# Kernel tuning notes

Measured on AMD Instinct MI355X. Metric: run time of the kernel, lower is better.

## Reference

```python
import jax, jax.numpy as jnp
import numpy as np

N_NODES = 50000
N_EDGES = 800000
IN_CH = 128
HID_CH = 256
N_GRAPHS = 500


def setup_inputs() -> dict:
    key = jax.random.key(0)
    k = jax.random.split(key, 8)
    x = jax.random.normal(k[0], (N_NODES, IN_CH), dtype=jnp.float32)
    edge_index = jax.random.randint(k[1], (2, N_EDGES), 0, N_NODES, dtype=jnp.int32)
    batch = jnp.sort(jax.random.randint(k[2], (N_NODES,), 0, N_GRAPHS, dtype=jnp.int32))
    # GCNConv weights (glorot-ish scaling) and zero biases, Linear fc is unused in forward
    W1 = jax.random.normal(k[3], (IN_CH, HID_CH), dtype=jnp.float32) / np.sqrt(IN_CH)
    b1 = jnp.zeros((HID_CH,), dtype=jnp.float32)
    W2 = jax.random.normal(k[4], (HID_CH, HID_CH), dtype=jnp.float32) / np.sqrt(HID_CH)
    b2 = jnp.zeros((HID_CH,), dtype=jnp.float32)
    return {"x": x, "W1": W1, "b1": b1, "W2": W2, "b2": b2,
            "edge_index": edge_index, "batch": batch}


def _gcn_conv(x, W, b, src, dst, norm, n_nodes):
    # x' = scatter_add_dst( norm_e * (x @ W)[src] ) + b   (self-loops already in src/dst)
    xw = x @ W                              # [N, H]
    msg = xw[src] * norm[:, None]           # [E+N, H]
    out = jax.ops.segment_sum(msg, dst, num_segments=n_nodes)
    return out + b


def reference(x, W1, b1, W2, b2, edge_index, batch):
    n = x.shape[0]
    # add self-loops (PyG GCNConv default)
    loop = jnp.arange(n, dtype=edge_index.dtype)
    src = jnp.concatenate([edge_index[0], loop])
    dst = jnp.concatenate([edge_index[1], loop])
    # symmetric normalization D^{-1/2} (A+I) D^{-1/2}; deg from dst counts
    deg = jax.ops.segment_sum(jnp.ones_like(dst, dtype=x.dtype), dst, num_segments=n)
    dis = jnp.where(deg > 0, jax.lax.rsqrt(deg), 0.0)
    norm = dis[src] * dis[dst]              # [E+N]

    h = jax.nn.relu(_gcn_conv(x, W1, b1, src, dst, norm, n))
    h = jax.nn.relu(_gcn_conv(h, W2, b2, src, dst, norm, n))

    # global_mean_pool over batch ids
    sums = jax.ops.segment_sum(h, batch, num_segments=N_GRAPHS)
    cnts = jax.ops.segment_sum(jnp.ones((n,), dtype=h.dtype), batch, num_segments=N_GRAPHS)
    return sums / jnp.maximum(cnts, 1.0)[:, None]
```

## Files before the change

### kernel.cpp

```cpp
#include <hip/hip_runtime.h>

#define HID 256
#define SLOTS 30
#define OVCAP 16384
#define NB 256
typedef unsigned short ushort_t;
typedef unsigned int uint_t;
typedef __attribute__((ext_vector_type(8))) short short8;
typedef __attribute__((ext_vector_type(4))) float f32x4;
typedef __attribute__((ext_vector_type(4))) unsigned short us4;
typedef __attribute__((ext_vector_type(8))) unsigned short us8;

__device__ __forceinline__ ushort_t f2b(float f) {
    uint_t u = __float_as_uint(f);
    u = u + 0x7fffu + ((u >> 16) & 1u);
    return (ushort_t)(u >> 16);
}

__global__ __launch_bounds__(256) void k_histprep(const int* __restrict__ dst,
                                                  int* __restrict__ hist,
                                                  int E, int CH, int NBKT,
                                                  const float* __restrict__ W1,
                                                  ushort_t* __restrict__ Wt1,
                                                  const float* __restrict__ W2,
                                                  ushort_t* __restrict__ Wt2, int p1b) {
    int bid = blockIdx.x;
    int tid = threadIdx.x;
    if (bid < NB) {
        __shared__ int h[256];
        h[tid] = 0;
        __syncthreads();
        int e0 = bid * CH;
        for (int it = tid; it < CH; it += 256) {
            int e = e0 + it;
            if (e < E) atomicAdd(&h[dst[e] >> 8], 1);
        }
        __syncthreads();
        if (tid < NBKT) hist[tid * NB + bid] = h[tid];
        return;
    }
    const float* W = (bid < NB + p1b) ? W1 : W2;
    ushort_t* Wt = (bid < NB + p1b) ? Wt1 : Wt2;
    int kg = (bid < NB + p1b) ? (bid - NB) : (bid - NB - p1b);
    int c = tid;
    float v = W[(size_t)kg * HID + c];
    int p = kg >> 6;
    int k = kg & 63;
    int byte_ = c * 128 + k * 2;
    int slot = byte_ >> 4;
    int sw = (slot & ~7) | ((slot ^ c) & 7);
    size_t dst_byte = (size_t)p * 32768 + ((size_t)sw << 4) + (byte_ & 15);
    Wt[dst_byte >> 1] = f2b(v);
}

__global__ __launch_bounds__(256) void k_scanb(const int* __restrict__ hist,
                                               int* __restrict__ offb,
                                               int* __restrict__ base,
                                               int* __restrict__ ovn, int NBKT) {
    __shared__ int s[256];
    int t = threadIdx.x;
    int sum = 0;
    if (t < NBKT) {
        const int* hp = hist + t * NB;
        for (int blk = 0; blk < NB; ++blk) sum += hp[blk];
    }
    s[t] = sum;
    __syncthreads();
#pragma unroll
    for (int d = 1; d < 256; d <<= 1) {
        int u = (t >= d) ? s[t - d] : 0;
        __syncthreads();
        s[t] += u;
        __syncthreads();
    }
    int myBase = s[t] - sum;
    if (t < NBKT) {
        base[t] = myBase;
        int run = myBase;
        const int* hp = hist + t * NB;
        int* op = offb + t * NB;
        for (int blk = 0; blk < NB; ++blk) { op[blk] = run; run += hp[blk]; }
    }
    if (t == 255) { base[NBKT] = s[255]; *ovn = 0; }
}

__global__ __launch_bounds__(256) void k_scatter(const int* __restrict__ src,
                                                 const int* __restrict__ dst,
                                                 const int* __restrict__ offb,
                                                 uint_t* __restrict__ scat,
                                                 int E, int CH) {
    __shared__ int h[256];
    int tid = threadIdx.x;
    int bid = blockIdx.x;
    h[tid] = 0;
    __syncthreads();
    int e0 = bid * CH;
    for (int it = tid; it < CH; it += 256) {
        int e = e0 + it;
        if (e < E) {
            int d = dst[e], sv = src[e];
            int b = d >> 8;
            int r = atomicAdd(&h[b], 1);
            scat[offb[b * NB + bid] + r] = ((uint_t)sv << 8) | (uint_t)(d & 255);
        }
    }
}

__global__ __launch_bounds__(256) void k_csr(const uint_t* __restrict__ scat,
                                             const int* __restrict__ base,
                                             ushort_t* __restrict__ csr2,
                                             float* __restrict__ dis,
                                             int* __restrict__ ovn,
                                             int2* __restrict__ ov,
                                             const float* __restrict__ x,
                                             ushort_t* __restrict__ xg, int n) {
    __shared__ ushort_t rows[256 * 32];
    __shared__ int rc[256];
    __shared__ float sdis[256];
    int tid = threadIdx.x;
    int b = blockIdx.x;
    rc[tid] = 0;
    uint4* r4 = (uint4*)rows;
#pragma unroll
    for (int k = tid; k < 1024; k += 256) r4[k] = make_uint4(0u, 0u, 0u, 0u);
    __syncthreads();
    int lo = base[b], hi = base[b + 1];
    for (int i = lo + tid; i < hi; i += 256) {
        uint_t p = scat[i];
        int local = (int)(p & 255u);
        int sv = (int)(p >> 8);
        int c = atomicAdd(&rc[local], 1);
        if (c < SLOTS) {
            rows[local * 32 + c] = (ushort_t)sv;
        } else {
            int q = atomicAdd(ovn, 1);
            if (q < OVCAP) ov[q] = make_int2(b * 256 + local, sv);
        }
    }
    __syncthreads();
    ((int*)(rows + tid * 32))[15] = rc[tid];
    float dv = rsqrtf((float)(rc[tid] + 1));
    sdis[tid] = dv;
    int node = b * 256 + tid;
    if (node < n) dis[node] = dv;
    __syncthreads();
    int node0 = b * 256;
    uint4* cg = (uint4*)csr2;
#pragma unroll
    for (int k = tid; k < 1024; k += 256) {
        int row = k >> 2, word = k & 3;
        if (node0 + row < n) cg[(size_t)(node0 + row) * 4 + word] = r4[row * 4 + word];
    }
#pragma unroll
    for (int c = 0; c < 16; ++c) {
        int u = c * 256 + tid;
        int rl = u >> 4;
        int j = u & 15;
        int node2 = node0 + rl;
        if (node2 < n) {
            float dvv = sdis[rl];
            const float4* p = (const float4*)(x + (size_t)node2 * 128 + j * 8);
            float4 v0 = p[0], v1 = p[1];
            us8 o;
            o[0] = f2b(v0.x * dvv); o[1] = f2b(v0.y * dvv);
            o[2] = f2b(v0.z * dvv); o[3] = f2b(v0.w * dvv);
            o[4] = f2b(v1.x * dvv); o[5] = f2b(v1.y * dvv);
            o[6] = f2b(v1.z * dvv); o[7] = f2b(v1.w * dvv);
            size_t dst = (size_t)(j >> 2) * ((size_t)n * 32) + (size_t)node2 * 32
                         + (size_t)(j & 3) * 8;
            *(us8*)(xg + dst) = o;
        }
    }
}

#define ACC8(r)                                                            \
    a0 += __uint_as_float((r).x << 16); a1 += __uint_as_float((r).x & 0xffff0000u); \
    a2 += __uint_as_float((r).y << 16); a3 += __uint_as_float((r).y & 0xffff0000u); \
    a4 += __uint_as_float((r).z << 16); a5 += __uint_as_float((r).z & 0xffff0000u); \
    a6 += __uint_as_float((r).w << 16); a7 += __uint_as_float((r).w & 0xffff0000u);

#define ACC8B(r)                                                           \
    b0 += __uint_as_float((r).x << 16); b1 += __uint_as_float((r).x & 0xffff0000u); \
    b2 += __uint_as_float((r).y << 16); b3 += __uint_as_float((r).y & 0xffff0000u); \
    b4 += __uint_as_float((r).z << 16); b5 += __uint_as_float((r).z & 0xffff0000u); \
    b6 += __uint_as_float((r).w << 16); b7 += __uint_as_float((r).w & 0xffff0000u);

template <int NG>
__global__ __launch_bounds__(256) void k_agg_g(const ushort_t* __restrict__ Yg,
                                               ushort_t* __restrict__ Z,
                                               const ushort_t* __restrict__ csr2,
                                               const int* __restrict__ ovn,
                                               const int2* __restrict__ ov,
                                               const float* __restrict__ dis, int n) {
    const int LOG = (NG == 8) ? 3 : 2;
    const int g = blockIdx.x & (NG - 1);
    const int chunk = blockIdx.x >> LOG;
    const int q = threadIdx.x >> 4;
    const int l16 = threadIdx.x & 15;
    const int par = l16 >> 2;
    const int sub = l16 & 3;
    const int v0 = chunk * 32 + q * 2;
    if (v0 >= n) return;
    const int v1 = v0 + 1;
    const bool has1 = (v1 < n);
    const uint4* Yb = (const uint4*)(Yg + (size_t)g * ((size_t)n * 32));
    const ushort_t* rowb0 = csr2 + (size_t)v0 * 32;
    const ushort_t* rowb1 = csr2 + (size_t)v1 * 32;
    const int deg0 = ((const int*)rowb0)[15];
    const int deg1 = has1 ? ((const int*)rowb1)[15] : 0;
    const int lim0 = min(deg0, SLOTS);
    const int lim1 = min(deg1, SLOTS);
    const int base = par * 8;
    us8 idx0 = *(const us8*)(rowb0 + base);
    us8 idx1 = {};
    if (has1) idx1 = *(const us8*)(rowb1 + base);
    uint4 self0 = make_uint4(0u, 0u, 0u, 0u), self1 = make_uint4(0u, 0u, 0u, 0u);
    if (par == 0) self0 = Yb[(uint_t)v0 * 4u + sub];
    if (has1 && par == 1) self1 = Yb[(uint_t)v1 * 4u + sub];

    const bool g0 = base < lim0;
    const bool g1 = has1 && (base < lim1);
    uint4 r0, r1, r2, r3, r4, r5, r6, r7;
    uint4 s0, s1, s2, s3, s4, s5, s6, s7;
    if (g0) {
        r0 = Yb[(uint_t)idx0[0] * 4u + sub]; r1 = Yb[(uint_t)idx0[1] * 4u + sub];
        r2 = Yb[(uint_t)idx0[2] * 4u + sub]; r3 = Yb[(uint_t)idx0[3] * 4u + sub];
        r4 = Yb[(uint_t)idx0[4] * 4u + sub]; r5 = Yb[(uint_t)idx0[5] * 4u + sub];
        r6 = Yb[(uint_t)idx0[6] * 4u + sub]; r7 = Yb[(uint_t)idx0[7] * 4u + sub];
    }
    if (g1) {
        s0 = Yb[(uint_t)idx1[0] * 4u + sub]; s1 = Yb[(uint_t)idx1[1] * 4u + sub];
        s2 = Yb[(uint_t)idx1[2] * 4u + sub]; s3 = Yb[(uint_t)idx1[3] * 4u + sub];
        s4 = Yb[(uint_t)idx1[4] * 4u + sub]; s5 = Yb[(uint_t)idx1[5] * 4u + sub];
        s6 = Yb[(uint_t)idx1[6] * 4u + sub]; s7 = Yb[(uint_t)idx1[7] * 4u + sub];
    }
    float a0 = 0.f, a1 = 0.f, a2 = 0.f, a3 = 0.f, a4 = 0.f, a5 = 0.f, a6 = 0.f, a7 = 0.f;
    float b0 = 0.f, b1 = 0.f, b2 = 0.f, b3 = 0.f, b4 = 0.f, b5 = 0.f, b6 = 0.f, b7 = 0.f;
    if (g0) {
        if (base + 0 < lim0) { ACC8(r0); }
        if (base + 1 < lim0) { ACC8(r1); }
        if (base + 2 < lim0) { ACC8(r2); }
        if (base + 3 < lim0) { ACC8(r3); }
        if (base + 4 < lim0) { ACC8(r4); }
        if (base + 5 < lim0) { ACC8(r5); }
        if (base + 6 < lim0) { ACC8(r6); }
        if (base + 7 < lim0) { ACC8(r7); }
    }
    if (g1) {
        if (base + 0 < lim1) { ACC8B(s0); }
        if (base + 1 < lim1) { ACC8B(s1); }
        if (base + 2 < lim1) { ACC8B(s2); }
        if (base + 3 < lim1) { ACC8B(s3); }
        if (base + 4 < lim1) { ACC8B(s4); }
        if (base + 5 < lim1) { ACC8B(s5); }
        if (base + 6 < lim1) { ACC8B(s6); }
        if (base + 7 < lim1) { ACC8B(s7); }
    }
    if (deg0 > SLOTS) {
        int m = min(*ovn, OVCAP);
        for (int i2 = par; i2 < m; i2 += 4) {
            int2 p = ov[i2];
            if (p.x == v0) { uint4 r = Yb[(uint_t)p.y * 4u + sub]; ACC8(r); }
        }
    }
    if (deg1 > SLOTS) {
        int m = min(*ovn, OVCAP);
        for (int i2 = par; i2 < m; i2 += 4) {
            int2 p = ov[i2];
            if (p.x == v1) { uint4 r = Yb[(uint_t)p.y * 4u + sub]; ACC8B(r); }
        }
    }
    a0 += __shfl_xor(a0, 4, 64); a1 += __shfl_xor(a1, 4, 64);
    a2 += __shfl_xor(a2, 4, 64); a3 += __shfl_xor(a3, 4, 64);
    a4 += __shfl_xor(a4, 4, 64); a5 += __shfl_xor(a5, 4, 64);
    a6 += __shfl_xor(a6, 4, 64); a7 += __shfl_xor(a7, 4, 64);
    a0 += __shfl_xor(a0, 8, 64); a1 += __shfl_xor(a1, 8, 64);
    a2 += __shfl_xor(a2, 8, 64); a3 += __shfl_xor(a3, 8, 64);
    a4 += __shfl_xor(a4, 8, 64); a5 += __shfl_xor(a5, 8, 64);
    a6 += __shfl_xor(a6, 8, 64); a7 += __shfl_xor(a7, 8, 64);
    b0 += __shfl_xor(b0, 4, 64); b1 += __shfl_xor(b1, 4, 64);
    b2 += __shfl_xor(b2, 4, 64); b3 += __shfl_xor(b3, 4, 64);
    b4 += __shfl_xor(b4, 4, 64); b5 += __shfl_xor(b5, 4, 64);
    b6 += __shfl_xor(b6, 4, 64); b7 += __shfl_xor(b7, 4, 64);
    b0 += __shfl_xor(b0, 8, 64); b1 += __shfl_xor(b1, 8, 64);
    b2 += __shfl_xor(b2, 8, 64); b3 += __shfl_xor(b3, 8, 64);
    b4 += __shfl_xor(b4, 8, 64); b5 += __shfl_xor(b5, 8, 64);
    b6 += __shfl_xor(b6, 8, 64); b7 += __shfl_xor(b7, 8, 64);
    if (par == 0) {
        ACC8(self0);
        float dv = dis[v0];
        us8 o;
        o[0] = f2b(a0 * dv); o[1] = f2b(a1 * dv); o[2] = f2b(a2 * dv); o[3] = f2b(a3 * dv);
        o[4] = f2b(a4 * dv); o[5] = f2b(a5 * dv); o[6] = f2b(a6 * dv); o[7] = f2b(a7 * dv);
        us8* zp = (us8*)(Z + (size_t)v0 * (NG * 32) + g * 32 + sub * 8);
        __builtin_nontemporal_store(o, zp);
    }
    if (has1 && par == 1) {
        ACC8B(self1);
        float dv = dis[v1];
        us8 o;
        o[0] = f2b(b0 * dv); o[1] = f2b(b1 * dv); o[2] = f2b(b2 * dv); o[3] = f2b(b3 * dv);
        o[4] = f2b(b4 * dv); o[5] = f2b(b5 * dv); o[6] = f2b(b6 * dv); o[7] = f2b(b7 * dv);
        us8* zp = (us8*)(Z + (size_t)v1 * (NG * 32) + g * 32 + sub * 8);
        __builtin_nontemporal_store(o, zp);
    }
}

template <int K, bool SCALE, bool OUTG>
__global__ __launch_bounds__(512) void k_gemm_mfma(const ushort_t* __restrict__ A,
                                                   const ushort_t* __restrict__ Wt,
                                                   const float* __restrict__ dis,
                                                   const float* __restrict__ bias,
                                                   ushort_t* __restrict__ Yout, int M) {
    __shared__ char lds[49152];
    char* As = lds;
    char* Bs = lds + 16384;
    const int tid = threadIdx.x;
    const int lane = tid & 63;
    const int w = tid >> 6;
    const int wm = w & 1;
    const int wn = w >> 1;
    const int row0 = blockIdx.x * 128;

    f32x4 acc[4][4];
#pragma unroll
    for (int i = 0; i < 4; ++i)
#pragma unroll
        for (int j = 0; j < 4; ++j) acc[i][j] = (f32x4){0.f, 0.f, 0.f, 0.f};

    for (int k0 = 0; k0 < K; k0 += 64) {
#pragma unroll
        for (int q = 0; q < 2; ++q) {
            int s = q * 512 + tid;
            int r = s >> 3;
            int kseg = (s & 7) ^ (r & 7);
            int row = row0 + r;
            if (row >= M) row = 0;
            const ushort_t* g = A + (size_t)row * K + k0 + kseg * 8;
            __builtin_amdgcn_global_load_lds((const uint_t*)g,
                                             (uint_t*)(As + q * 8192 + w * 1024), 16, 0, 0);
        }
        const ushort_t* gp = Wt + (size_t)(k0 >> 6) * (256 * 64);
#pragma unroll
        for (int q = 0; q < 4; ++q) {
            int s = q * 512 + tid;
            __builtin_amdgcn_global_load_lds((const uint_t*)(gp + (size_t)s * 8),
                                             (uint_t*)(Bs + q * 8192 + w * 1024), 16, 0, 0);
        }
        __syncthreads();
#pragma unroll
        for (int k32 = 0; k32 < 2; ++k32) {
            const int ksl = k32 * 4 + (lane >> 4);
            short8 wf[4], xf[4];
#pragma unroll
            for (int nn = 0; nn < 4; ++nn) {
                int col = wn * 64 + nn * 16 + (lane & 15);
                int slot = col * 8 + (ksl ^ (col & 7));
                wf[nn] = *(const short8*)(Bs + slot * 16);
            }
#pragma unroll
            for (int m = 0; m < 4; ++m) {
                int row = wm * 64 + m * 16 + (lane & 15);
                int slot = row * 8 + (ksl ^ (row & 7));
                xf[m] = *(const short8*)(As + slot * 16);
            }
#pragma unroll
            for (int nn = 0; nn < 4; ++nn)
#pragma unroll
                for (int m = 0; m < 4; ++m)
                    acc[nn][m] = __builtin_amdgcn_mfma_f32_16x16x32_bf16(wf[nn], xf[m],
                                                                         acc[nn][m], 0, 0, 0);
        }
        __syncthreads();
    }
    const int m_lo = lane & 15, c_hi = lane >> 4;
#pragma unroll
    for (int m = 0; m < 4; ++m) {
        int row = row0 + wm * 64 + m * 16 + m_lo;
        if (row < M) {
            float dv = SCALE ? dis[row] : 1.f;
#pragma unroll
            for (int nn = 0; nn < 4; ++nn) {
                int c0 = wn * 64 + nn * 16 + c_hi * 4;
                float4 bb = *(const float4*)(bias + c0);
                us4 o;
                o[0] = f2b(fmaxf(acc[nn][m][0] + bb.x, 0.f) * dv);
                o[1] = f2b(fmaxf(acc[nn][m][1] + bb.y, 0.f) * dv);
                o[2] = f2b(fmaxf(acc[nn][m][2] + bb.z, 0.f) * dv);
                o[3] = f2b(fmaxf(acc[nn][m][3] + bb.w, 0.f) * dv);
                size_t dst = OUTG
                    ? ((size_t)(c0 >> 5) * ((size_t)M * 32) + (size_t)row * 32 + (c0 & 31))
                    : ((size_t)row * HID + c0);
                *(us4*)(Yout + dst) = o;
            }
        }
    }
}

__global__ __launch_bounds__(256) void k_pool2(const ushort_t* __restrict__ H,
                                               const int* __restrict__ batch,
                                               float* __restrict__ out, int n) {
    __shared__ int se[2];
    int g = blockIdx.x;
    if (threadIdx.x < 2) {
        int tgt = g + (int)threadIdx.x;
        int lo = 0, hi = n;
        while (lo < hi) { int mid = (lo + hi) >> 1; if (batch[mid] < tgt) lo = mid + 1; else hi = mid; }
        se[threadIdx.x] = lo;
    }
    __syncthreads();
    int s = se[0], e = se[1];
    int c = threadIdx.x;
    float sum = 0.f;
    for (int i = s; i < e; ++i)
        sum += __uint_as_float(((uint_t)H[(size_t)i * HID + c]) << 16);
    out[(size_t)g * HID + c] = sum / (float)max(e - s, 1);
}

extern "C" void kernel_launch(void* const* d_in, const int* in_sizes, int n_in,
                              void* d_out, int out_size, void* d_ws, size_t ws_size,
                              hipStream_t stream) {
    const float* x = (const float*)d_in[0];
    const float* W1 = (const float*)d_in[1];
    const float* b1 = (const float*)d_in[2];
    const float* W2 = (const float*)d_in[3];
    const float* b2 = (const float*)d_in[4];
    const int* ei = (const int*)d_in[5];
    const int* batch = (const int*)d_in[6];
    float* out = (float*)d_out;

    const int N = in_sizes[6];
    const int E = in_sizes[5] / 2;
    const int K1 = in_sizes[0] / N;
    const int G = out_size / HID;
    (void)n_in; (void)ws_size; (void)K1;

    char* w = (char*)d_ws;
    int* ovn = (int*)(w + 0);
    int2* ov = (int2*)(w + 64);
    ushort_t* csr2 = (ushort_t*)(w + 131136);
    float* dis = (float*)(w + 3331136);
    ushort_t* Wt1 = (ushort_t*)(w + 3531136);
    ushort_t* Wt2 = (ushort_t*)(w + 3596672);
    ushort_t* Xg = (ushort_t*)(w + 3727744);
    ushort_t* Z1 = (ushort_t*)(w + 16527744);
    ushort_t* H1g = (ushort_t*)(w + 29327744);
    ushort_t* Z2 = (ushort_t*)(w + 3727744);
    ushort_t* H2 = (ushort_t*)(w + 29327744);
    int* hist = (int*)(w + 54927744);
    int* offb = (int*)(w + 55128448);
    int* base = (int*)(w + 55329152);
    uint_t* scat = (uint_t*)(w + 55330048);

    const int NBKT = (N + 255) >> 8;
    const int CH = (E + NB - 1) / NB;
    k_histprep<<<NB + K1 + HID, 256, 0, stream>>>(ei + E, hist, E, CH, NBKT,
                                                  W1, Wt1, W2, Wt2, K1);
    k_scanb<<<1, 256, 0, stream>>>(hist, offb, base, ovn, NBKT);
    k_scatter<<<NB, 256, 0, stream>>>(ei, ei + E, offb, scat, E, CH);
    k_csr<<<NBKT, 256, 0, stream>>>(scat, base, csr2, dis, ovn, ov, x, Xg, N);

    int gblk = (N + 127) / 128;
    const int chunks32 = (N + 31) / 32;
    k_agg_g<4><<<4 * chunks32, 256, 0, stream>>>(Xg, Z1, csr2, ovn, ov, dis, N);
    k_gemm_mfma<128, true, true><<<gblk, 512, 0, stream>>>(Z1, Wt1, dis, b1, H1g, N);
    k_agg_g<8><<<8 * chunks32, 256, 0, stream>>>(H1g, Z2, csr2, ovn, ov, dis, N);
    k_gemm_mfma<256, false, false><<<gblk, 512, 0, stream>>>(Z2, Wt2, dis, b2, H2, N);

    k_pool2<<<G, 256, 0, stream>>>(H2, batch, out, N);
}
```

Before: 202.8 us.

## Sort nodes by degree and process one node per 16-lane group in aggregation

Adds a degree histogram in k_csr plus two new kernels (a scan and a scatter) that build a permutation of nodes sorted into degree bins. The aggregation kernels now handle one node per 16-lane group taken from this permutation, instead of two consecutive nodes per group. The aim is to cut warp divergence and load imbalance from varying degrees, so that lanes in a wave finish at similar times. In exchange it adds launches and an extra indirection through perm, halves the per-thread work, and gives up the locality of consecutive node ids for Z writes and self reads.

```diff
diff --git a/kernel.cpp b/kernel.cpp
--- a/kernel.cpp
+++ b/kernel.cpp
@@ -113,13 +113,16 @@
                                              int* __restrict__ ovn,
                                              int2* __restrict__ ov,
                                              const float* __restrict__ x,
-                                             ushort_t* __restrict__ xg, int n) {
+                                             ushort_t* __restrict__ xg,
+                                             int* __restrict__ dhist, int n) {
     __shared__ ushort_t rows[256 * 32];
     __shared__ int rc[256];
     __shared__ float sdis[256];
+    __shared__ int dh[32];
     int tid = threadIdx.x;
     int b = blockIdx.x;
     rc[tid] = 0;
+    if (tid < 32) dh[tid] = 0;
     uint4* r4 = (uint4*)rows;
 #pragma unroll
     for (int k = tid; k < 1024; k += 256) r4[k] = make_uint4(0u, 0u, 0u, 0u);
@@ -142,8 +145,12 @@
     float dv = rsqrtf((float)(rc[tid] + 1));
     sdis[tid] = dv;
     int node = b * 256 + tid;
-    if (node < n) dis[node] = dv;
-    __syncthreads();
+    if (node < n) {
+        dis[node] = dv;
+        atomicAdd(&dh[min(rc[tid], 31)], 1);
+    }
+    __syncthreads();
+    if (tid < 32) dhist[b * 32 + tid] = dh[tid];
     int node0 = b * 256;
     uint4* cg = (uint4*)csr2;
 #pragma unroll
@@ -173,17 +180,49 @@
     }
 }
 
+__global__ __launch_bounds__(256) void k_dscan(const int* __restrict__ dhist,
+                                               int* __restrict__ doffb, int NBKT) {
+    __shared__ int s[32];
+    int t = threadIdx.x;
+    if (t < 32) {
+        int sum = 0;
+        for (int b = 0; b < NBKT; ++b) sum += dhist[b * 32 + t];
+        s[t] = sum;
+    }
+    __syncthreads();
+    if (t == 0) {
+        int run = 0;
+        for (int d = 0; d < 32; ++d) { int c = s[d]; s[d] = run; run += c; }
+    }
+    __syncthreads();
+    if (t < 32) {
+        int run = s[t];
+        for (int b = 0; b < NBKT; ++b) { doffb[t * NBKT + b] = run; run += dhist[b * 32 + t]; }
+    }
+}
+
+__global__ __launch_bounds__(256) void k_dscat(const ushort_t* __restrict__ csr2,
+                                               const int* __restrict__ doffb,
+                                               int* __restrict__ perm, int n, int NBKT) {
+    __shared__ int dh[32];
+    int tid = threadIdx.x;
+    int b = blockIdx.x;
+    if (tid < 32) dh[tid] = 0;
+    __syncthreads();
+    int node = b * 256 + tid;
+    if (node < n) {
+        int deg = ((const int*)csr2)[node * 16 + 15];
+        int bin = min(deg, 31);
+        int r = atomicAdd(&dh[bin], 1);
+        perm[doffb[bin * NBKT + b] + r] = node;
+    }
+}
+
 #define ACC8(r)                                                            \
     a0 += __uint_as_float((r).x << 16); a1 += __uint_as_float((r).x & 0xffff0000u); \
     a2 += __uint_as_float((r).y << 16); a3 += __uint_as_float((r).y & 0xffff0000u); \
     a4 += __uint_as_float((r).z << 16); a5 += __uint_as_float((r).z & 0xffff0000u); \
     a6 += __uint_as_float((r).w << 16); a7 += __uint_as_float((r).w & 0xffff0000u);
-
-#define ACC8B(r)                                                           \
-    b0 += __uint_as_float((r).x << 16); b1 += __uint_as_float((r).x & 0xffff0000u); \
-    b2 += __uint_as_float((r).y << 16); b3 += __uint_as_float((r).y & 0xffff0000u); \
-    b4 += __uint_as_float((r).z << 16); b5 += __uint_as_float((r).z & 0xffff0000u); \
-    b6 += __uint_as_float((r).w << 16); b7 += __uint_as_float((r).w & 0xffff0000u);
 
 template <int NG>
 __global__ __launch_bounds__(256) void k_agg_g(const ushort_t* __restrict__ Yg,
@@ -191,83 +230,50 @@
                                                const ushort_t* __restrict__ csr2,
                                                const int* __restrict__ ovn,
                                                const int2* __restrict__ ov,
-                                               const float* __restrict__ dis, int n) {
+                                               const float* __restrict__ dis,
+                                               const int* __restrict__ perm, int n) {
     const int LOG = (NG == 8) ? 3 : 2;
     const int g = blockIdx.x & (NG - 1);
     const int chunk = blockIdx.x >> LOG;
     const int q = threadIdx.x >> 4;
     const int l16 = threadIdx.x & 15;
+    const int pi = chunk * 16 + q;
+    if (pi >= n) return;
+    const int v = perm[pi];
     const int par = l16 >> 2;
     const int sub = l16 & 3;
-    const int v0 = chunk * 32 + q * 2;
-    if (v0 >= n) return;
-    const int v1 = v0 + 1;
-    const bool has1 = (v1 < n);
     const uint4* Yb = (const uint4*)(Yg + (size_t)g * ((size_t)n * 32));
-    const ushort_t* rowb0 = csr2 + (size_t)v0 * 32;
-    const ushort_t* rowb1 = csr2 + (size_t)v1 * 32;
-    const int deg0 = ((const int*)rowb0)[15];
-    const int deg1 = has1 ? ((const int*)rowb1)[15] : 0;
-    const int lim0 = min(deg0, SLOTS);
-    const int lim1 = min(deg1, SLOTS);
+    const ushort_t* rowb = csr2 + (size_t)v * 32;
+    const int deg = ((const int*)rowb)[15];
+    const int lim = min(deg, SLOTS);
     const int base = par * 8;
-    us8 idx0 = *(const us8*)(rowb0 + base);
-    us8 idx1 = {};
-    if (has1) idx1 = *(const us8*)(rowb1 + base);
-    uint4 self0 = make_uint4(0u, 0u, 0u, 0u), self1 = make_uint4(0u, 0u, 0u, 0u);
-    if (par == 0) self0 = Yb[(uint_t)v0 * 4u + sub];
-    if (has1 && par == 1) self1 = Yb[(uint_t)v1 * 4u + sub];
-
-    const bool g0 = base < lim0;
-    const bool g1 = has1 && (base < lim1);
-    uint4 r0, r1, r2, r3, r4, r5, r6, r7;
-    uint4 s0, s1, s2, s3, s4, s5, s6, s7;
-    if (g0) {
-        r0 = Yb[(uint_t)idx0[0] * 4u + sub]; r1 = Yb[(uint_t)idx0[1] * 4u + sub];
-        r2 = Yb[(uint_t)idx0[2] * 4u + sub]; r3 = Yb[(uint_t)idx0[3] * 4u + sub];
-        r4 = Yb[(uint_t)idx0[4] * 4u + sub]; r5 = Yb[(uint_t)idx0[5] * 4u + sub];
-        r6 = Yb[(uint_t)idx0[6] * 4u + sub]; r7 = Yb[(uint_t)idx0[7] * 4u + sub];
-    }
-    if (g1) {
-        s0 = Yb[(uint_t)idx1[0] * 4u + sub]; s1 = Yb[(uint_t)idx1[1] * 4u + sub];
-        s2 = Yb[(uint_t)idx1[2] * 4u + sub]; s3 = Yb[(uint_t)idx1[3] * 4u + sub];
-        s4 = Yb[(uint_t)idx1[4] * 4u + sub]; s5 = Yb[(uint_t)idx1[5] * 4u + sub];
-        s6 = Yb[(uint_t)idx1[6] * 4u + sub]; s7 = Yb[(uint_t)idx1[7] * 4u + sub];
-    }
+    uint4 self = make_uint4(0u, 0u, 0u, 0u);
+    if (par == 0) self = Yb[(uint_t)v * 4u + sub];
     float a0 = 0.f, a1 = 0.f, a2 = 0.f, a3 = 0.f, a4 = 0.f, a5 = 0.f, a6 = 0.f, a7 = 0.f;
-    float b0 = 0.f, b1 = 0.f, b2 = 0.f, b3 = 0.f, b4 = 0.f, b5 = 0.f, b6 = 0.f, b7 = 0.f;
-    if (g0) {
-        if (base + 0 < lim0) { ACC8(r0); }
-        if (base + 1 < lim0) { ACC8(r1); }
-        if (base + 2 < lim0) { ACC8(r2); }
-        if (base + 3 < lim0) { ACC8(r3); }
-        if (base + 4 < lim0) { ACC8(r4); }
-        if (base + 5 < lim0) { ACC8(r5); }
-        if (base + 6 < lim0) { ACC8(r6); }
-        if (base + 7 < lim0) { ACC8(r7); }
-    }
-    if (g1) {
-        if (base + 0 < lim1) { ACC8B(s0); }
-        if (base + 1 < lim1) { ACC8B(s1); }
-        if (base + 2 < lim1) { ACC8B(s2); }
-        if (base + 3 < lim1) { ACC8B(s3); }
-        if (base + 4 < lim1) { ACC8B(s4); }
-        if (base + 5 < lim1) { ACC8B(s5); }
-        if (base + 6 < lim1) { ACC8B(s6); }
-        if (base + 7 < lim1) { ACC8B(s7); }
-    }
-    if (deg0 > SLOTS) {
+    if (base < lim) {
+        us8 idx = *(const us8*)(rowb + base);
+        uint4 r0 = Yb[(uint_t)idx[0] * 4u + sub];
+        uint4 r1 = Yb[(uint_t)idx[1] * 4u + sub];
+        uint4 r2 = Yb[(uint_t)idx[2] * 4u + sub];
+        uint4 r3 = Yb[(uint_t)idx[3] * 4u + sub];
+        uint4 r4 = Yb[(uint_t)idx[4] * 4u + sub];
+        uint4 r5 = Yb[(uint_t)idx[5] * 4u + sub];
+        uint4 r6 = Yb[(uint_t)idx[6] * 4u + sub];
+        uint4 r7 = Yb[(uint_t)idx[7] * 4u + sub];
+        if (base + 0 < lim) { ACC8(r0); }
+        if (base + 1 < lim) { ACC8(r1); }
+        if (base + 2 < lim) { ACC8(r2); }
+        if (base + 3 < lim) { ACC8(r3); }
+        if (base + 4 < lim) { ACC8(r4); }
+        if (base + 5 < lim) { ACC8(r5); }
+        if (base + 6 < lim) { ACC8(r6); }
+        if (base + 7 < lim) { ACC8(r7); }
+    }
+    if (deg > SLOTS) {
         int m = min(*ovn, OVCAP);
         for (int i2 = par; i2 < m; i2 += 4) {
             int2 p = ov[i2];
-            if (p.x == v0) { uint4 r = Yb[(uint_t)p.y * 4u + sub]; ACC8(r); }
-        }
-    }
-    if (deg1 > SLOTS) {
-        int m = min(*ovn, OVCAP);
-        for (int i2 = par; i2 < m; i2 += 4) {
-            int2 p = ov[i2];
-            if (p.x == v1) { uint4 r = Yb[(uint_t)p.y * 4u + sub]; ACC8B(r); }
+            if (p.x == v) { uint4 r = Yb[(uint_t)p.y * 4u + sub]; ACC8(r); }
         }
     }
     a0 += __shfl_xor(a0, 4, 64); a1 += __shfl_xor(a1, 4, 64);
@@ -278,30 +284,13 @@
     a2 += __shfl_xor(a2, 8, 64); a3 += __shfl_xor(a3, 8, 64);
     a4 += __shfl_xor(a4, 8, 64); a5 += __shfl_xor(a5, 8, 64);
     a6 += __shfl_xor(a6, 8, 64); a7 += __shfl_xor(a7, 8, 64);
-    b0 += __shfl_xor(b0, 4, 64); b1 += __shfl_xor(b1, 4, 64);
-    b2 += __shfl_xor(b2, 4, 64); b3 += __shfl_xor(b3, 4, 64);
-    b4 += __shfl_xor(b4, 4, 64); b5 += __shfl_xor(b5, 4, 64);
-    b6 += __shfl_xor(b6, 4, 64); b7 += __shfl_xor(b7, 4, 64);
-    b0 += __shfl_xor(b0, 8, 64); b1 += __shfl_xor(b1, 8, 64);
-    b2 += __shfl_xor(b2, 8, 64); b3 += __shfl_xor(b3, 8, 64);
-    b4 += __shfl_xor(b4, 8, 64); b5 += __shfl_xor(b5, 8, 64);
-    b6 += __shfl_xor(b6, 8, 64); b7 += __shfl_xor(b7, 8, 64);
     if (par == 0) {
-        ACC8(self0);
-        float dv = dis[v0];
+        ACC8(self);
+        float dv = dis[v];
         us8 o;
         o[0] = f2b(a0 * dv); o[1] = f2b(a1 * dv); o[2] = f2b(a2 * dv); o[3] = f2b(a3 * dv);
         o[4] = f2b(a4 * dv); o[5] = f2b(a5 * dv); o[6] = f2b(a6 * dv); o[7] = f2b(a7 * dv);
-        us8* zp = (us8*)(Z + (size_t)v0 * (NG * 32) + g * 32 + sub * 8);
-        __builtin_nontemporal_store(o, zp);
-    }
-    if (has1 && par == 1) {
-        ACC8B(self1);
-        float dv = dis[v1];
-        us8 o;
-        o[0] = f2b(b0 * dv); o[1] = f2b(b1 * dv); o[2] = f2b(b2 * dv); o[3] = f2b(b3 * dv);
-        o[4] = f2b(b4 * dv); o[5] = f2b(b5 * dv); o[6] = f2b(b6 * dv); o[7] = f2b(b7 * dv);
-        us8* zp = (us8*)(Z + (size_t)v1 * (NG * 32) + g * 32 + sub * 8);
+        us8* zp = (us8*)(Z + (size_t)v * (NG * 32) + g * 32 + sub * 8);
         __builtin_nontemporal_store(o, zp);
     }
 }
@@ -433,7 +422,7 @@
     const int E = in_sizes[5] / 2;
     const int K1 = in_sizes[0] / N;
     const int G = out_size / HID;
-    (void)n_in; (void)ws_size; (void)K1;
+    (void)n_in; (void)ws_size;
 
     char* w = (char*)d_ws;
     int* ovn = (int*)(w + 0);
@@ -451,6 +440,9 @@
     int* offb = (int*)(w + 55128448);
     int* base = (int*)(w + 55329152);
     uint_t* scat = (uint_t*)(w + 55330048);
+    int* dhist = (int*)(w + 58530048);
+    int* doffb = (int*)(w + 58555136);
+    int* perm = (int*)(w + 58580224);
 
     const int NBKT = (N + 255) >> 8;
     const int CH = (E + NB - 1) / NB;
@@ -458,13 +450,15 @@
                                                   W1, Wt1, W2, Wt2, K1);
     k_scanb<<<1, 256, 0, stream>>>(hist, offb, base, ovn, NBKT);
     k_scatter<<<NB, 256, 0, stream>>>(ei, ei + E, offb, scat, E, CH);
-    k_csr<<<NBKT, 256, 0, stream>>>(scat, base, csr2, dis, ovn, ov, x, Xg, N);
+    k_csr<<<NBKT, 256, 0, stream>>>(scat, base, csr2, dis, ovn, ov, x, Xg, dhist, N);
+    k_dscan<<<1, 256, 0, stream>>>(dhist, doffb, NBKT);
+    k_dscat<<<NBKT, 256, 0, stream>>>(csr2, doffb, perm, N, NBKT);
 
     int gblk = (N + 127) / 128;
-    const int chunks32 = (N + 31) / 32;
-    k_agg_g<4><<<4 * chunks32, 256, 0, stream>>>(Xg, Z1, csr2, ovn, ov, dis, N);
+    const int chunks16 = (N + 15) / 16;
+    k_agg_g<4><<<4 * chunks16, 256, 0, stream>>>(Xg, Z1, csr2, ovn, ov, dis, perm, N);
     k_gemm_mfma<128, true, true><<<gblk, 512, 0, stream>>>(Z1, Wt1, dis, b1, H1g, N);
-    k_agg_g<8><<<8 * chunks32, 256, 0, stream>>>(H1g, Z2, csr2, ovn, ov, dis, N);
+    k_agg_g<8><<<8 * chunks16, 256, 0, stream>>>(H1g, Z2, csr2, ovn, ov, dis, perm, N);
     k_gemm_mfma<256, false, false><<<gblk, 512, 0, stream>>>(Z2, Wt2, dis, b2, H2, N);
 
     k_pool2<<<G, 256, 0, stream>>>(H2, batch, out, N);
```

Result: slower. 261.3 us (+28.9%).
